# Performance work log

Hardware: AMD Instinct MI355X
Metric: run time of the kernel (lower is better)

Reference implementation:

```python
import jax, jax.numpy as jnp
import numpy as np

K = 3
K2 = K * K
STRIDE, PAD, DIL = 1, 1, 1


def conv2d(x, w, b, stride, pad, dil):
    out = jax.lax.conv_general_dilated(
        x, w, (stride, stride), [(pad, pad), (pad, pad)],
        rhs_dilation=(dil, dil),
        dimension_numbers=("NCHW", "OIHW", "NCHW"))
    return out + b[None, :, None, None]


def deform_sample(img, py, px):
    """Bilinear sample with zero padding outside.
    img: [C,H,W]; py,px: [K2,Ho,Wo] float sample coords -> [C,K2,Ho,Wo]."""
    C, H, W = img.shape
    y0 = jnp.floor(py)
    x0 = jnp.floor(px)
    acc = jnp.zeros((C,) + py.shape, img.dtype)
    for dy in (0.0, 1.0):
        for dx in (0.0, 1.0):
            yi = y0 + dy
            xi = x0 + dx
            wgt = (1.0 - jnp.abs(py - yi)) * (1.0 - jnp.abs(px - xi))
            valid = (yi >= 0) & (yi < H) & (xi >= 0) & (xi < W)
            yc = jnp.clip(yi, 0, H - 1).astype(jnp.int32)
            xc = jnp.clip(xi, 0, W - 1).astype(jnp.int32)
            v = img[:, yc, xc]  # gather -> [C,K2,Ho,Wo]
            acc = acc + v * (wgt * valid)[None]
    return acc


def setup_inputs() -> dict:
    key = jax.random.key(0)
    k1, k2, k3, k4 = jax.random.split(key, 4)
    Cin, Cout = 64, 64
    x = jax.random.normal(k1, (4, Cin, 128, 128), jnp.float32)
    # small offset-conv weights so learned offsets stay in a few-pixel range
    w_off = jax.random.normal(k2, (3 * K2, Cin, K, K), jnp.float32) * 0.01
    b_off = jnp.zeros((3 * K2,), jnp.float32)
    # folded (BN-fused) deform conv weight/bias
    w = jax.random.normal(k3, (Cout, Cin, K, K), jnp.float32) * (1.0 / np.sqrt(Cin * K2))
    b = jax.random.normal(k4, (Cout,), jnp.float32) * 0.1
    return {"x": x, "w_off": w_off, "b_off": b_off, "w": w, "b": b}


def reference(x, w_off, b_off, w, b):
    N, C, H, W = x.shape
    # offset/mask conv -> chunk into (o1, o2, mask), cat offsets, sigmoid mask
    om = conv2d(x, w_off, b_off, STRIDE, PAD, DIL)  # [N, 27, Ho, Wo]
    o1, o2, m = jnp.split(om, 3, axis=1)
    offset = jnp.concatenate([o1, o2], axis=1)      # [N, 2*K2, Ho, Wo]
    mask = jax.nn.sigmoid(m)                        # [N, K2, Ho, Wo]
    Ho, Wo = offset.shape[2], offset.shape[3]
    # torchvision layout: per kernel tap (dy, dx) pairs
    off = offset.reshape(N, K2, 2, Ho, Wo)
    dy, dx = off[:, :, 0], off[:, :, 1]
    hk, wk = jnp.meshgrid(jnp.arange(K), jnp.arange(K), indexing="ij")
    base_y = ((jnp.arange(Ho) * STRIDE - PAD)[None, :, None]
              + (hk.reshape(K2) * DIL)[:, None, None])  # [K2,Ho,1]
    base_x = ((jnp.arange(Wo) * STRIDE - PAD)[None, None, :]
              + (wk.reshape(K2) * DIL)[:, None, None])  # [K2,1,Wo]
    py = base_y.astype(x.dtype) + dy                    # [N,K2,Ho,Wo]
    px = base_x.astype(x.dtype) + dx
    sampled = jax.vmap(deform_sample)(x, py, px)        # [N,C,K2,Ho,Wo]
    sampled = sampled * mask[:, None]
    out = jnp.einsum("ock,nckhw->nohw", w.reshape(w.shape[0], C, K2), sampled)
    out = out + b[None, :, None, None]
    return jax.nn.relu(out)
```

## Files before the change

kernel.cpp:

```cpp
#include <hip/hip_runtime.h>
#include <math.h>

#define N_ 4
#define C_ 64
#define H_ 128
#define W_ 128
#define HW_ (H_ * W_)
#define K2_ 9
#define COUT 64
#define CK 576
#define TP 16
#define NT 2
#define SST 584
#define GUARD 128

typedef __bf16 bf16x8 __attribute__((ext_vector_type(8)));
typedef __bf16 bf16x2 __attribute__((ext_vector_type(2)));
typedef float floatx4 __attribute__((ext_vector_type(4)));
typedef float floatx2 __attribute__((ext_vector_type(2)));
typedef unsigned uint2v __attribute__((ext_vector_type(2)));

__device__ __forceinline__ float bflo(unsigned u) {
    return __builtin_bit_cast(float, u << 16);
}
__device__ __forceinline__ float bfhi(unsigned u) {
    return __builtin_bit_cast(float, u & 0xffff0000u);
}

__global__ __launch_bounds__(256) void prep_kernel(const float* __restrict__ x,
                                                   const float* __restrict__ w,
                                                   const float* __restrict__ w_off,
                                                   __bf16* __restrict__ xT,
                                                   __bf16* __restrict__ w2,
                                                   __bf16* __restrict__ w_off2) {
    __shared__ float s_t[64][33];
    int t = threadIdx.x;
    int bx = blockIdx.x;
    int y = blockIdx.y, n = blockIdx.z;
    if (bx < 4) {
        int x0 = bx * 32;
        int c = t >> 2, seg = (t & 3) * 8;
        const float* src = x + (((size_t)n * C_ + c) * H_ + y) * W_ + x0 + seg;
        floatx4 v0 = *(const floatx4*)src;
        floatx4 v1 = *(const floatx4*)(src + 4);
#pragma unroll
        for (int j = 0; j < 4; ++j) { s_t[c][seg + j] = v0[j]; s_t[c][seg + 4 + j] = v1[j]; }
        __syncthreads();
        int xl = t >> 3, cb = (t & 7) * 8;
        bf16x8 o;
#pragma unroll
        for (int j = 0; j < 8; ++j) o[j] = (__bf16)s_t[cb + j][xl];
        *(bf16x8*)(xT + (((size_t)n * H_ + y) * W_ + x0 + xl) * C_ + cb) = o;
    } else {
        int linear = (n * 128 + y) * 256 + t;
        if (linear < COUT * CK) {
            int o = linear / CK, r = linear - o * CK;
            int k = r >> 6, c = r & 63;
            w2[linear] = (__bf16)w[(o * C_ + c) * K2_ + k];
        }
        if (linear < 32 * CK) {
            int o = linear / CK, r = linear - o * CK;
            int k = r >> 6, c = r & 63;
            w_off2[linear] = (o < 27) ? (__bf16)w_off[(o * C_ + c) * K2_ + k] : (__bf16)0.f;
        }
    }
}

__global__ __launch_bounds__(256) void fused_kernel(const __bf16* __restrict__ xT,
                                                    const __bf16* __restrict__ w2,
                                                    const __bf16* __restrict__ w_off2,
                                                    const float* __restrict__ b_off,
                                                    const float* __restrict__ b,
                                                    float* __restrict__ out) {
    __shared__ __align__(16) __bf16 s_x[NT][TP * SST];
    __shared__ float s_om[NT][2][32 * TP];
    __shared__ floatx4 s_w4[NT][K2_ * TP];
    __shared__ int s_pix[NT][K2_ * TP];

    int t = threadIdx.x;
    int pixbase = blockIdx.x * (TP * NT);
    int wo0 = pixbase & (W_ - 1);
    int ho  = (pixbase >> 7) & (H_ - 1);
    int n   = pixbase >> 14;
    const __bf16* xn = xT + (size_t)n * HW_ * C_;

    int lane = t & 63;
    int wv   = t >> 6;
    int half = lane >> 5;
    int li   = lane & 31;
    int q    = lane >> 4;
    int col  = lane & 15;

    {
        uint2v ua[18];
        int tl = wv >> 1;
        int rb = (wv & 1) * 36 + half;
#pragma unroll
        for (int j = 0; j < 18; ++j) {
            int r  = rb + 2 * j;
            int k  = r >> 3;
            int p0 = (r & 7) * 2;
            int kh = k / 3, kw = k - kh * 3;
            int y  = ho - 1 + kh;
            int yc = min(max(y, 0), H_ - 1);
            int xx = wo0 + 16 * tl + p0 - 1 + kw;
            int pix = yc * W_ + xx;
            ua[j] = *((const uint2v*)(xn + (ptrdiff_t)pix * C_) + li);
        }
#pragma unroll
        for (int j = 0; j < 18; ++j) {
            int r  = rb + 2 * j;
            int k  = r >> 3;
            int p0 = (r & 7) * 2;
            int kh = k / 3, kw = k - kh * 3;
            int y  = ho - 1 + kh;
            int xx = wo0 + 16 * tl + p0 - 1 + kw;
            bool vy = (unsigned)y < (unsigned)H_;
            int myxx = xx + (li >> 4);
            bool valid = vy && ((unsigned)myxx < (unsigned)W_);
            uint2v v = ua[j];
            v.x = valid ? v.x : 0u;
            v.y = valid ? v.y : 0u;
            int p = p0 + (li >> 4);
            *(uint2v*)&s_x[tl][p * SST + k * 64 + 4 * (li & 15)] = v;
        }
    }
    __syncthreads();

    {
        int r = wv >> 1;
        int h = wv & 1;
        const __bf16* ar = w_off2 + (size_t)(16 * r + col) * CK + h * 288 + q * 8;
        const __bf16* b0 = s_x[0] + col * SST + h * 288 + q * 8;
        const __bf16* b1 = s_x[1] + col * SST + h * 288 + q * 8;
        floatx4 acc0 = {0.f, 0.f, 0.f, 0.f}, acc1 = {0.f, 0.f, 0.f, 0.f};
#pragma unroll
        for (int it = 0; it < 9; ++it) {
            bf16x8 a   = *(const bf16x8*)(ar + 32 * it);
            bf16x8 bb0 = *(const bf16x8*)(b0 + 32 * it);
            bf16x8 bb1 = *(const bf16x8*)(b1 + 32 * it);
            acc0 = __builtin_amdgcn_mfma_f32_16x16x32_bf16(a, bb0, acc0, 0, 0, 0);
            acc1 = __builtin_amdgcn_mfma_f32_16x16x32_bf16(a, bb1, acc1, 0, 0, 0);
        }
#pragma unroll
        for (int rr = 0; rr < 4; ++rr) {
            s_om[0][h][(16 * r + q * 4 + rr) * TP + col] = acc0[rr];
            s_om[1][h][(16 * r + q * 4 + rr) * TP + col] = acc1[rr];
        }
    }
    __syncthreads();

#pragma unroll
    for (int it2 = 0; it2 < 2; ++it2) {
        int i = it2 * 256 + t;
        if (i < NT * K2_ * TP) {
            int tl = (i >= 144);
            int P  = i - 144 * tl;
            int k  = P >> 4;
            int pp = P & 15;
            float dy = s_om[tl][0][(2 * k) * TP + pp]     + s_om[tl][1][(2 * k) * TP + pp]     + b_off[2 * k];
            float dx = s_om[tl][0][(2 * k + 1) * TP + pp] + s_om[tl][1][(2 * k + 1) * TP + pp] + b_off[2 * k + 1];
            float mm = s_om[tl][0][(18 + k) * TP + pp]    + s_om[tl][1][(18 + k) * TP + pp]    + b_off[18 + k];
            float msk = 1.f / (1.f + expf(-mm));
            int kh = k / 3, kw = k - kh * 3;
            float py = (float)(ho - 1 + kh) + dy;
            float px = (float)(wo0 + 16 * tl + pp - 1 + kw) + dx;
            float yf = floorf(py), xf = floorf(px);
            float fy = py - yf, fx = px - xf;
            int y0 = (int)yf, x0 = (int)xf;
            float wy0 = ((unsigned)y0 < (unsigned)H_)       ? 1.f - fy : 0.f;
            float wy1 = ((unsigned)(y0 + 1) < (unsigned)H_) ? fy       : 0.f;
            float wx0 = ((unsigned)x0 < (unsigned)W_)       ? 1.f - fx : 0.f;
            float wx1 = ((unsigned)(x0 + 1) < (unsigned)W_) ? fx      : 0.f;
            int y0c = min(max(y0, 0), H_ - 2);
            int x0c = min(max(x0, 0), W_ - 2);
            float t0 = (y0 == y0c) ? wy0 : ((y0 + 1 == y0c) ? wy1 : 0.f);
            float t1 = (y0 == y0c) ? wy1 : ((y0 == y0c + 1) ? wy0 : 0.f);
            float u0 = (x0 == x0c) ? wx0 : ((x0 + 1 == x0c) ? wx1 : 0.f);
            float u1 = (x0 == x0c) ? wx1 : ((x0 == x0c + 1) ? wx0 : 0.f);
            floatx4 w4 = { t0 * u0 * msk, t0 * u1 * msk, t1 * u0 * msk, t1 * u1 * msk };
            s_w4[tl][P] = w4;
            s_pix[tl][P] = y0c * W_ + x0c;
        }
    }
    __syncthreads();

    {
        int Pb = wv * 36 + half;
        unsigned buf[4][4];
#pragma unroll
        for (int g = 0; g < 3; ++g) {
            int pix = s_pix[0][Pb + 2 * g];
            const unsigned* bp = (const unsigned*)(xn + (size_t)pix * C_) + li;
            buf[g][0] = bp[0];
            buf[g][1] = bp[32];
            buf[g][2] = bp[W_ * 32];
            buf[g][3] = bp[W_ * 32 + 32];
        }
#pragma unroll
        for (int g = 0; g < 36; ++g) {
            if (g < 33) {
                int gn = g + 3;
                int tln = (gn >= 18);
                int pix = s_pix[tln][Pb + 2 * (gn - 18 * tln)];
                const unsigned* bp = (const unsigned*)(xn + (size_t)pix * C_) + li;
                unsigned* d = buf[gn & 3];
                d[0] = bp[0];
                d[1] = bp[32];
                d[2] = bp[W_ * 32];
                d[3] = bp[W_ * 32 + 32];
            }
            int tl = (g >= 18);
            int P = Pb + 2 * (g - 18 * tl);
            floatx4 w4 = s_w4[tl][P];
            const unsigned* a = buf[g & 3];
            float lo = w4[0] * bflo(a[0]) + w4[1] * bflo(a[1])
                     + w4[2] * bflo(a[2]) + w4[3] * bflo(a[3]);
            float hi = w4[0] * bfhi(a[0]) + w4[1] * bfhi(a[1])
                     + w4[2] * bfhi(a[2]) + w4[3] * bfhi(a[3]);
            floatx2 fv = {lo, hi};
            bf16x2 bv = __builtin_convertvector(fv, bf16x2);
            int k = P >> 4, p = P & 15;
            *(unsigned*)&s_x[tl][p * SST + k * 64 + 2 * li] = __builtin_bit_cast(unsigned, bv);
        }
    }
    __syncthreads();

    {
        const __bf16* ar = w2 + (size_t)(16 * wv + col) * CK + q * 8;
        const __bf16* b0 = s_x[0] + col * SST + q * 8;
        const __bf16* b1 = s_x[1] + col * SST + q * 8;
        floatx4 acc0 = {0.f, 0.f, 0.f, 0.f}, acc1 = {0.f, 0.f, 0.f, 0.f};
        bf16x8 a_cur = *(const bf16x8*)ar;
#pragma unroll
        for (int it = 0; it < 18; ++it) {
            bf16x8 a_nxt;
            if (it < 17) a_nxt = *(const bf16x8*)(ar + 32 * (it + 1));
            bf16x8 bb0 = *(const bf16x8*)(b0 + 32 * it);
            bf16x8 bb1 = *(const bf16x8*)(b1 + 32 * it);
            acc0 = __builtin_amdgcn_mfma_f32_16x16x32_bf16(a_cur, bb0, acc0, 0, 0, 0);
            acc1 = __builtin_amdgcn_mfma_f32_16x16x32_bf16(a_cur, bb1, acc1, 0, 0, 0);
            a_cur = a_nxt;
        }
#pragma unroll
        for (int r = 0; r < 4; ++r) {
            int o = 16 * wv + q * 4 + r;
            float bias = b[o];
            float* ob = out + (((size_t)n * COUT + o) * H_ + ho) * W_ + wo0;
            ob[col]      = fmaxf(acc0[r] + bias, 0.f);
            ob[16 + col] = fmaxf(acc1[r] + bias, 0.f);
        }
    }
}

extern "C" void kernel_launch(void* const* d_in, const int* in_sizes, int n_in,
                              void* d_out, int out_size, void* d_ws, size_t ws_size,
                              hipStream_t stream) {
    const float* x     = (const float*)d_in[0];
    const float* w_off = (const float*)d_in[1];
    const float* b_off = (const float*)d_in[2];
    const float* w     = (const float*)d_in[3];
    const float* b     = (const float*)d_in[4];
    float* out = (float*)d_out;

    __bf16* xT     = (__bf16*)d_ws + GUARD;
    __bf16* w2     = xT + (size_t)N_ * HW_ * C_ + GUARD;
    __bf16* w_off2 = w2 + (size_t)COUT * CK;

    prep_kernel<<<dim3(5, 128, 4), 256, 0, stream>>>(x, w, w_off, xT, w2, w_off2);

    int nblocks = N_ * H_ * W_ / (TP * NT);
    fused_kernel<<<nblocks, 256, 0, stream>>>(xT, w2, w_off2, b_off, b, out);
}
```

Before: 120.2 us.

## Widen bilinear gather to 8-byte loads with deeper prefetch pipeline

Restructures the deformable bilinear sampling loop so each lane loads 4 channels (8 bytes) per corner instead of 2, with 16 lanes covering a pixel's channels and 4 sample points per wave step. The loop count drops from 36 to 18 iterations, pixel indices are hoisted into registers, and the prefetch depth grows from 3 to 8 samples in flight. The goal is fewer, wider global memory transactions and more latency hiding for the gather. In exchange it uses more registers for the deeper buffer, which may reduce occupancy, and writes 8-byte chunks to shared memory.

After: 125.3 us. 1.04x slower.

```diff
diff --git a/kernel.cpp b/kernel.cpp
--- a/kernel.cpp
+++ b/kernel.cpp
@@ -15,6 +15,7 @@
 #define GUARD 128
 
 typedef __bf16 bf16x8 __attribute__((ext_vector_type(8)));
+typedef __bf16 bf16x4 __attribute__((ext_vector_type(4)));
 typedef __bf16 bf16x2 __attribute__((ext_vector_type(2)));
 typedef float floatx4 __attribute__((ext_vector_type(4)));
 typedef float floatx2 __attribute__((ext_vector_type(2)));
@@ -186,43 +187,50 @@
     __syncthreads();
 
     {
-        int Pb = wv * 36 + half;
-        unsigned buf[4][4];
-#pragma unroll
-        for (int g = 0; g < 3; ++g) {
-            int pix = s_pix[0][Pb + 2 * g];
-            const unsigned* bp = (const unsigned*)(xn + (size_t)pix * C_) + li;
-            buf[g][0] = bp[0];
-            buf[g][1] = bp[32];
-            buf[g][2] = bp[W_ * 32];
-            buf[g][3] = bp[W_ * 32 + 32];
-        }
-#pragma unroll
-        for (int g = 0; g < 36; ++g) {
-            if (g < 33) {
-                int gn = g + 3;
-                int tln = (gn >= 18);
-                int pix = s_pix[tln][Pb + 2 * (gn - 18 * tln)];
-                const unsigned* bp = (const unsigned*)(xn + (size_t)pix * C_) + li;
-                unsigned* d = buf[gn & 3];
-                d[0] = bp[0];
-                d[1] = bp[32];
-                d[2] = bp[W_ * 32];
-                d[3] = bp[W_ * 32 + 32];
+        int qw   = lane >> 4;
+        int li16 = lane & 15;
+        int Pb   = wv * 36;
+        int pixv[18];
+#pragma unroll
+        for (int i = 0; i < 18; ++i) {
+            int tl_ = (i >= 9);
+            int P_  = Pb + (i - 9 * tl_) * 4 + qw;
+            pixv[i] = s_pix[tl_][P_];
+        }
+        uint2v buf[8][4];
+#define ISSUE(ii)                                                                         \
+        do {                                                                              \
+            const uint2v* bp = (const uint2v*)(xn + (ptrdiff_t)pixv[(ii)] * C_) + li16;   \
+            uint2v* d = buf[(ii) & 7];                                                    \
+            d[0] = bp[0];                                                                 \
+            d[1] = bp[16];                                                                \
+            d[2] = bp[16 * W_];                                                           \
+            d[3] = bp[16 * W_ + 16];                                                      \
+        } while (0)
+#pragma unroll
+        for (int i = 0; i < 8; ++i) ISSUE(i);
+#pragma unroll
+        for (int i = 0; i < 18; ++i) {
+            int tl = (i >= 9);
+            int P  = Pb + (i - 9 * tl) * 4 + qw;
+            floatx4 w4 = s_w4[tl][P];
+            const uint2v* a = buf[i & 7];
+            floatx2 sa = {0.f, 0.f}, sb = {0.f, 0.f};
+#pragma unroll
+            for (int tp = 0; tp < 4; ++tp) {
+                unsigned ux = a[tp].x, uy = a[tp].y;
+                floatx2 pa = {bflo(ux), bfhi(ux)};
+                floatx2 pb = {bflo(uy), bfhi(uy)};
+                sa += pa * w4[tp];
+                sb += pb * w4[tp];
             }
-            int tl = (g >= 18);
-            int P = Pb + 2 * (g - 18 * tl);
-            floatx4 w4 = s_w4[tl][P];
-            const unsigned* a = buf[g & 3];
-            float lo = w4[0] * bflo(a[0]) + w4[1] * bflo(a[1])
-                     + w4[2] * bflo(a[2]) + w4[3] * bflo(a[3]);
-            float hi = w4[0] * bfhi(a[0]) + w4[1] * bfhi(a[1])
-                     + w4[2] * bfhi(a[2]) + w4[3] * bfhi(a[3]);
-            floatx2 fv = {lo, hi};
-            bf16x2 bv = __builtin_convertvector(fv, bf16x2);
+            if (i < 10) ISSUE(i + 8);
+            floatx4 fv = {sa[0], sa[1], sb[0], sb[1]};
+            bf16x4 bv = __builtin_convertvector(fv, bf16x4);
             int k = P >> 4, p = P & 15;
-            *(unsigned*)&s_x[tl][p * SST + k * 64 + 2 * li] = __builtin_bit_cast(unsigned, bv);
-        }
+            *(uint2v*)&s_x[tl][p * SST + k * 64 + 4 * li16] = __builtin_bit_cast(uint2v, bv);
+        }
+#undef ISSUE
     }
     __syncthreads();
 
```

## Double block size to 512 threads, splitting each tile across separate wave groups

Applied to the files above, without the earlier changes.

The fused deformable-conv kernel now launches 512 threads per block, 8 waves, where the first four waves handle pixel tile 0 and the last four handle tile 1. Each wave does half the previous per-thread work: fewer staging loads, one MFMA accumulator instead of two, and half as many bilinear gather iterations. The offset-weight stage now runs in a single pass over 288 threads instead of a two-iteration loop. Launch bounds request 6 blocks of 512 threads per CU, which caps register use, so the aim is more latency hiding at the cost of possible spills and lower LDS-limited occupancy.

After: 142.0 us. 1.18x slower.

```diff
diff --git a/kernel.cpp b/kernel.cpp
--- a/kernel.cpp
+++ b/kernel.cpp
@@ -66,12 +66,12 @@
     }
 }
 
-__global__ __launch_bounds__(256) void fused_kernel(const __bf16* __restrict__ xT,
-                                                    const __bf16* __restrict__ w2,
-                                                    const __bf16* __restrict__ w_off2,
-                                                    const float* __restrict__ b_off,
-                                                    const float* __restrict__ b,
-                                                    float* __restrict__ out) {
+__global__ __launch_bounds__(512, 6) void fused_kernel(const __bf16* __restrict__ xT,
+                                                       const __bf16* __restrict__ w2,
+                                                       const __bf16* __restrict__ w_off2,
+                                                       const float* __restrict__ b_off,
+                                                       const float* __restrict__ b,
+                                                       float* __restrict__ out) {
     __shared__ __align__(16) __bf16 s_x[NT][TP * SST];
     __shared__ float s_om[NT][2][32 * TP];
     __shared__ floatx4 s_w4[NT][K2_ * TP];
@@ -90,13 +90,14 @@
     int li   = lane & 31;
     int q    = lane >> 4;
     int col  = lane & 15;
-
-    {
-        uint2v ua[18];
-        int tl = wv >> 1;
-        int rb = (wv & 1) * 36 + half;
-#pragma unroll
-        for (int j = 0; j < 18; ++j) {
+    int tl   = wv >> 2;
+    int w4i  = wv & 3;
+
+    {
+        uint2v ua[9];
+        int rb = w4i * 18 + half;
+#pragma unroll
+        for (int j = 0; j < 9; ++j) {
             int r  = rb + 2 * j;
             int k  = r >> 3;
             int p0 = (r & 7) * 2;
@@ -108,7 +109,7 @@
             ua[j] = *((const uint2v*)(xn + (ptrdiff_t)pix * C_) + li);
         }
 #pragma unroll
-        for (int j = 0; j < 18; ++j) {
+        for (int j = 0; j < 9; ++j) {
             int r  = rb + 2 * j;
             int k  = r >> 3;
             int p0 = (r & 7) * 2;
@@ -128,69 +129,62 @@
     __syncthreads();
 
     {
-        int r = wv >> 1;
+        int r = (wv >> 1) & 1;
         int h = wv & 1;
         const __bf16* ar = w_off2 + (size_t)(16 * r + col) * CK + h * 288 + q * 8;
-        const __bf16* b0 = s_x[0] + col * SST + h * 288 + q * 8;
-        const __bf16* b1 = s_x[1] + col * SST + h * 288 + q * 8;
-        floatx4 acc0 = {0.f, 0.f, 0.f, 0.f}, acc1 = {0.f, 0.f, 0.f, 0.f};
+        const __bf16* bb = s_x[tl] + col * SST + h * 288 + q * 8;
+        floatx4 acc = {0.f, 0.f, 0.f, 0.f};
 #pragma unroll
         for (int it = 0; it < 9; ++it) {
-            bf16x8 a   = *(const bf16x8*)(ar + 32 * it);
-            bf16x8 bb0 = *(const bf16x8*)(b0 + 32 * it);
-            bf16x8 bb1 = *(const bf16x8*)(b1 + 32 * it);
-            acc0 = __builtin_amdgcn_mfma_f32_16x16x32_bf16(a, bb0, acc0, 0, 0, 0);
-            acc1 = __builtin_amdgcn_mfma_f32_16x16x32_bf16(a, bb1, acc1, 0, 0, 0);
+            bf16x8 a  = *(const bf16x8*)(ar + 32 * it);
+            bf16x8 bv = *(const bf16x8*)(bb + 32 * it);
+            acc = __builtin_amdgcn_mfma_f32_16x16x32_bf16(a, bv, acc, 0, 0, 0);
         }
 #pragma unroll
         for (int rr = 0; rr < 4; ++rr) {
-            s_om[0][h][(16 * r + q * 4 + rr) * TP + col] = acc0[rr];
-            s_om[1][h][(16 * r + q * 4 + rr) * TP + col] = acc1[rr];
-        }
-    }
-    __syncthreads();
-
-#pragma unroll
-    for (int it2 = 0; it2 < 2; ++it2) {
-        int i = it2 * 256 + t;
-        if (i < NT * K2_ * TP) {
-            int tl = (i >= 144);
-            int P  = i - 144 * tl;
-            int k  = P >> 4;
-            int pp = P & 15;
-            float dy = s_om[tl][0][(2 * k) * TP + pp]     + s_om[tl][1][(2 * k) * TP + pp]     + b_off[2 * k];
-            float dx = s_om[tl][0][(2 * k + 1) * TP + pp] + s_om[tl][1][(2 * k + 1) * TP + pp] + b_off[2 * k + 1];
-            float mm = s_om[tl][0][(18 + k) * TP + pp]    + s_om[tl][1][(18 + k) * TP + pp]    + b_off[18 + k];
-            float msk = 1.f / (1.f + expf(-mm));
-            int kh = k / 3, kw = k - kh * 3;
-            float py = (float)(ho - 1 + kh) + dy;
-            float px = (float)(wo0 + 16 * tl + pp - 1 + kw) + dx;
-            float yf = floorf(py), xf = floorf(px);
-            float fy = py - yf, fx = px - xf;
-            int y0 = (int)yf, x0 = (int)xf;
-            float wy0 = ((unsigned)y0 < (unsigned)H_)       ? 1.f - fy : 0.f;
-            float wy1 = ((unsigned)(y0 + 1) < (unsigned)H_) ? fy       : 0.f;
-            float wx0 = ((unsigned)x0 < (unsigned)W_)       ? 1.f - fx : 0.f;
-            float wx1 = ((unsigned)(x0 + 1) < (unsigned)W_) ? fx      : 0.f;
-            int y0c = min(max(y0, 0), H_ - 2);
-            int x0c = min(max(x0, 0), W_ - 2);
-            float t0 = (y0 == y0c) ? wy0 : ((y0 + 1 == y0c) ? wy1 : 0.f);
-            float t1 = (y0 == y0c) ? wy1 : ((y0 == y0c + 1) ? wy0 : 0.f);
-            float u0 = (x0 == x0c) ? wx0 : ((x0 + 1 == x0c) ? wx1 : 0.f);
-            float u1 = (x0 == x0c) ? wx1 : ((x0 == x0c + 1) ? wx0 : 0.f);
-            floatx4 w4 = { t0 * u0 * msk, t0 * u1 * msk, t1 * u0 * msk, t1 * u1 * msk };
-            s_w4[tl][P] = w4;
-            s_pix[tl][P] = y0c * W_ + x0c;
-        }
-    }
-    __syncthreads();
-
-    {
-        int Pb = wv * 36 + half;
+            s_om[tl][h][(16 * r + q * 4 + rr) * TP + col] = acc[rr];
+        }
+    }
+    __syncthreads();
+
+    if (t < NT * K2_ * TP) {
+        int i = t;
+        int tc = (i >= 144);
+        int P  = i - 144 * tc;
+        int k  = P >> 4;
+        int pp = P & 15;
+        float dy = s_om[tc][0][(2 * k) * TP + pp]     + s_om[tc][1][(2 * k) * TP + pp]     + b_off[2 * k];
+        float dx = s_om[tc][0][(2 * k + 1) * TP + pp] + s_om[tc][1][(2 * k + 1) * TP + pp] + b_off[2 * k + 1];
+        float mm = s_om[tc][0][(18 + k) * TP + pp]    + s_om[tc][1][(18 + k) * TP + pp]    + b_off[18 + k];
+        float msk = 1.f / (1.f + expf(-mm));
+        int kh = k / 3, kw = k - kh * 3;
+        float py = (float)(ho - 1 + kh) + dy;
+        float px = (float)(wo0 + 16 * tc + pp - 1 + kw) + dx;
+        float yf = floorf(py), xf = floorf(px);
+        float fy = py - yf, fx = px - xf;
+        int y0 = (int)yf, x0 = (int)xf;
+        float wy0 = ((unsigned)y0 < (unsigned)H_)       ? 1.f - fy : 0.f;
+        float wy1 = ((unsigned)(y0 + 1) < (unsigned)H_) ? fy       : 0.f;
+        float wx0 = ((unsigned)x0 < (unsigned)W_)       ? 1.f - fx : 0.f;
+        float wx1 = ((unsigned)(x0 + 1) < (unsigned)W_) ? fx      : 0.f;
+        int y0c = min(max(y0, 0), H_ - 2);
+        int x0c = min(max(x0, 0), W_ - 2);
+        float t0 = (y0 == y0c) ? wy0 : ((y0 + 1 == y0c) ? wy1 : 0.f);
+        float t1 = (y0 == y0c) ? wy1 : ((y0 == y0c + 1) ? wy0 : 0.f);
+        float u0 = (x0 == x0c) ? wx0 : ((x0 + 1 == x0c) ? wx1 : 0.f);
+        float u1 = (x0 == x0c) ? wx1 : ((x0 == x0c + 1) ? wx0 : 0.f);
+        floatx4 w4 = { t0 * u0 * msk, t0 * u1 * msk, t1 * u0 * msk, t1 * u1 * msk };
+        s_w4[tc][P] = w4;
+        s_pix[tc][P] = y0c * W_ + x0c;
+    }
+    __syncthreads();
+
+    {
+        int Pb = w4i * 36 + half;
         unsigned buf[4][4];
 #pragma unroll
         for (int g = 0; g < 3; ++g) {
-            int pix = s_pix[0][Pb + 2 * g];
+            int pix = s_pix[tl][Pb + 2 * g];
             const unsigned* bp = (const unsigned*)(xn + (size_t)pix * C_) + li;
             buf[g][0] = bp[0];
             buf[g][1] = bp[32];
@@ -198,11 +192,10 @@
             buf[g][3] = bp[W_ * 32 + 32];
         }
 #pragma unroll
-        for (int g = 0; g < 36; ++g) {
-            if (g < 33) {
+        for (int g = 0; g < 18; ++g) {
+            if (g < 15) {
                 int gn = g + 3;
-                int tln = (gn >= 18);
-                int pix = s_pix[tln][Pb + 2 * (gn - 18 * tln)];
+                int pix = s_pix[tl][Pb + 2 * gn];
                 const unsigned* bp = (const unsigned*)(xn + (size_t)pix * C_) + li;
                 unsigned* d = buf[gn & 3];
                 d[0] = bp[0];
@@ -210,8 +203,7 @@
                 d[2] = bp[W_ * 32];
                 d[3] = bp[W_ * 32 + 32];
             }
-            int tl = (g >= 18);
-            int P = Pb + 2 * (g - 18 * tl);
+            int P = Pb + 2 * g;
             floatx4 w4 = s_w4[tl][P];
             const unsigned* a = buf[g & 3];
             float lo = w4[0] * bflo(a[0]) + w4[1] * bflo(a[1])
@@ -227,28 +219,24 @@
     __syncthreads();
 
     {
-        const __bf16* ar = w2 + (size_t)(16 * wv + col) * CK + q * 8;
-        const __bf16* b0 = s_x[0] + col * SST + q * 8;
-        const __bf16* b1 = s_x[1] + col * SST + q * 8;
-        floatx4 acc0 = {0.f, 0.f, 0.f, 0.f}, acc1 = {0.f, 0.f, 0.f, 0.f};
+        const __bf16* ar = w2 + (size_t)(16 * w4i + col) * CK + q * 8;
+        const __bf16* bb = s_x[tl] + col * SST + q * 8;
+        floatx4 acc = {0.f, 0.f, 0.f, 0.f};
         bf16x8 a_cur = *(const bf16x8*)ar;
 #pragma unroll
         for (int it = 0; it < 18; ++it) {
             bf16x8 a_nxt;
             if (it < 17) a_nxt = *(const bf16x8*)(ar + 32 * (it + 1));
-            bf16x8 bb0 = *(const bf16x8*)(b0 + 32 * it);
-            bf16x8 bb1 = *(const bf16x8*)(b1 + 32 * it);
-            acc0 = __builtin_amdgcn_mfma_f32_16x16x32_bf16(a_cur, bb0, acc0, 0, 0, 0);
-            acc1 = __builtin_amdgcn_mfma_f32_16x16x32_bf16(a_cur, bb1, acc1, 0, 0, 0);
+            bf16x8 bv = *(const bf16x8*)(bb + 32 * it);
+            acc = __builtin_amdgcn_mfma_f32_16x16x32_bf16(a_cur, bv, acc, 0, 0, 0);
             a_cur = a_nxt;
         }
 #pragma unroll
         for (int r = 0; r < 4; ++r) {
-            int o = 16 * wv + q * 4 + r;
+            int o = 16 * w4i + q * 4 + r;
             float bias = b[o];
-            float* ob = out + (((size_t)n * COUT + o) * H_ + ho) * W_ + wo0;
-            ob[col]      = fmaxf(acc0[r] + bias, 0.f);
-            ob[16 + col] = fmaxf(acc1[r] + bias, 0.f);
+            float* ob = out + (((size_t)n * COUT + o) * H_ + ho) * W_ + wo0 + 16 * tl;
+            ob[col] = fmaxf(acc[r] + bias, 0.f);
         }
     }
 }
@@ -270,5 +258,5 @@
     prep_kernel<<<dim3(5, 128, 4), 256, 0, stream>>>(x, w, w_off, xT, w2, w_off2);
 
     int nblocks = N_ * H_ * W_ / (TP * NT);
-    fused_kernel<<<nblocks, 256, 0, stream>>>(xT, w2, w_off2, b_off, b, out);
-}
+    fused_kernel<<<nblocks, 512, 0, stream>>>(xT, w2, w_off2, b_off, b, out);
+}
```
